# Performance work log

Hardware: AMD Instinct MI355X
Metric: run time of the kernel (lower is better)

## Reference

```python
import jax, jax.numpy as jnp
import numpy as np

B, T, C, H = 8, 2048, 1024, 128  # batch, seq (== block_size), n_embd, head_size


def setup_inputs() -> dict:
    key = jax.random.key(0)
    ks = jax.random.split(key, 4)
    s = 1.0 / np.sqrt(C)  # keep logits sane for softmax
    return {
        "embedded_data": jax.random.normal(ks[0], (B, T, C), dtype=jnp.float32),
        "Wq": jax.random.normal(ks[1], (C, H), dtype=jnp.float32) * s,
        "bq": jnp.zeros((H,), dtype=jnp.float32),
        "Wk": jax.random.normal(ks[2], (C, H), dtype=jnp.float32) * s,
        "bk": jnp.zeros((H,), dtype=jnp.float32),
        "Wv": jax.random.normal(ks[3], (C, H), dtype=jnp.float32) * s,
        "bv": jnp.zeros((H,), dtype=jnp.float32),
    }


def reference(embedded_data, Wq, bq, Wk, bk, Wv, bv):
    Bc, Tc, Cc = embedded_data.shape
    q = embedded_data @ Wq + bq                      # [B,T,H]
    k = embedded_data @ Wk + bk                      # [B,T,H]
    v = embedded_data @ Wv + bv                      # [B,T,H]
    # NOTE: source scales by C**-0.5 (input embed dim), not head_size**-0.5
    wei = jnp.einsum("bqh,bkh->bqk", q, k) * (Cc ** -0.5)  # [B,T,T]
    causal = jnp.tril(jnp.ones((Tc, Tc), dtype=bool))
    wei = jnp.where(causal, wei, -jnp.inf)
    wei = jax.nn.softmax(wei, axis=-1)
    # dropout(p=0.2) is identity in eval mode
    out = jnp.einsum("bqk,bkh->bqh", wei, v)         # [B,T,H]
    return out
```

## Files before the change

### kernel.cpp

```cpp
#include <hip/hip_runtime.h>
#include <cstdint>
#include <cstddef>

typedef __bf16 bf16x8 __attribute__((ext_vector_type(8)));
typedef float f32x4 __attribute__((ext_vector_type(4)));

#define B_ 8
#define T_ 2048
#define C_ 1024
#define H_ 128

#define QSC 0.045084220027780106f

__device__ __forceinline__ unsigned short f2bf(float f) {
    __bf16 h = (__bf16)f;
    return *(unsigned short*)&h;
}
__device__ __forceinline__ float bf2f(unsigned short u) {
    union { unsigned int i; float f; } x; x.i = ((unsigned int)u) << 16;
    return x.f;
}

__device__ __forceinline__ void gload16(void* lds, const void* g) {
    __builtin_amdgcn_global_load_lds(
        (const __attribute__((address_space(1))) unsigned int*)g,
        (__attribute__((address_space(3))) unsigned int*)lds, 16, 0, 0);
}

__global__ __launch_bounds__(256) void prep_w(
    const float* __restrict__ Wq, const float* __restrict__ Wk,
    const float* __restrict__ Wv, unsigned short* __restrict__ wt)
{
    int gid = blockIdx.x * 256 + threadIdx.x;
    int which = gid >> 14;
    int rem = gid & 16383;
    int n = rem >> 7;
    int kc = rem & 127;
    const float* W = which == 0 ? Wq : (which == 1 ? Wk : Wv);
    unsigned short tmp[8];
    #pragma unroll
    for (int i = 0; i < 8; ++i) tmp[i] = f2bf(W[(size_t)(kc * 8 + i) * H_ + n]);
    *(uint4*)&wt[((size_t)which * H_ + n) * C_ + kc * 8] = *(uint4*)tmp;
}

__global__ __launch_bounds__(256) void proj_kernel(
    const float* __restrict__ x, const unsigned short* __restrict__ wt,
    const float* __restrict__ bq, const float* __restrict__ bk,
    const float* __restrict__ bv,
    unsigned short* __restrict__ qo, unsigned short* __restrict__ ko,
    unsigned short* __restrict__ vo)
{
    const int which = blockIdx.y;
    const float* bias = which == 0 ? bq : (which == 1 ? bk : bv);

    __shared__ float xs[2][64 * 64];
    __shared__ unsigned short ws2[2][128 * 64];

    const int tid = threadIdx.x;
    const int w = tid >> 6, l = tid & 63, g = l >> 4, lc = l & 15;
    const int wm = w & 1, wn = w >> 1;
    const int m0 = blockIdx.x * 64;

    const unsigned short* wbase = &wt[(size_t)which * H_ * C_];

    f32x4 acc[2][4];
    #pragma unroll
    for (int im = 0; im < 2; ++im)
        #pragma unroll
        for (int jn = 0; jn < 4; ++jn) acc[im][jn] = f32x4{0.f, 0.f, 0.f, 0.f};

    auto stage = [&](int buf, int kc2) {
        const int kb = kc2 * 64;
        #pragma unroll
        for (int jj = 0; jj < 4; ++jj) {
            int slot = w * 256 + jj * 64 + l;
            int r = slot >> 3, cs = slot & 7;
            gload16(&ws2[buf][(w * 256 + jj * 64) * 8],
                    &wbase[(size_t)r * C_ + kb + ((cs ^ (r & 7)) * 8)]);
        }
        #pragma unroll
        for (int jj = 0; jj < 4; ++jj) {
            int slot = w * 256 + jj * 64 + l;
            int r = slot >> 4, cs = slot & 15;
            gload16(&xs[buf][(w * 256 + jj * 64) * 4],
                    &x[(size_t)(m0 + r) * C_ + kb + ((cs ^ (r & 15)) * 4)]);
        }
    };

    stage(0, 0);
    __syncthreads();

    int cur = 0;
    for (int kc = 0; kc < 16; ++kc) {
        if (kc < 15) stage(cur ^ 1, kc + 1);
        #pragma unroll
        for (int ks = 0; ks < 2; ++ks) {
            bf16x8 a[2], b[4];
            #pragma unroll
            for (int im = 0; im < 2; ++im) {
                int row = wm * 32 + im * 16 + lc;
                int u0 = ks * 8 + g * 2;
                f32x4 lo = *(const f32x4*)&xs[cur][(row * 16 + (u0 ^ (row & 15))) * 4];
                f32x4 hi = *(const f32x4*)&xs[cur][(row * 16 + ((u0 + 1) ^ (row & 15))) * 4];
                bf16x8 af;
                af[0] = (__bf16)lo[0]; af[1] = (__bf16)lo[1];
                af[2] = (__bf16)lo[2]; af[3] = (__bf16)lo[3];
                af[4] = (__bf16)hi[0]; af[5] = (__bf16)hi[1];
                af[6] = (__bf16)hi[2]; af[7] = (__bf16)hi[3];
                a[im] = af;
            }
            #pragma unroll
            for (int jn = 0; jn < 4; ++jn) {
                int n = wn * 64 + jn * 16 + lc;
                b[jn] = *(const bf16x8*)&ws2[cur][(n * 8 + ((ks * 4 + g) ^ (n & 7))) * 8];
            }
            #pragma unroll
            for (int im = 0; im < 2; ++im)
                #pragma unroll
                for (int jn = 0; jn < 4; ++jn)
                    acc[im][jn] = __builtin_amdgcn_mfma_f32_16x16x32_bf16(
                        a[im], b[jn], acc[im][jn], 0, 0, 0);
        }
        __syncthreads();
        cur ^= 1;
    }

    unsigned short* eb = (unsigned short*)&xs[0][0];
    if (which != 2) {
        const float osc = (which == 0) ? QSC : 1.0f;
        #pragma unroll
        for (int jn = 0; jn < 4; ++jn) {
            int n = wn * 64 + jn * 16 + lc;
            float bval = bias[n];
            #pragma unroll
            for (int im = 0; im < 2; ++im)
                #pragma unroll
                for (int r = 0; r < 4; ++r) {
                    int ml = wm * 32 + im * 16 + g * 4 + r;
                    eb[ml * 128 + n] = f2bf((acc[im][jn][r] + bval) * osc);
                }
        }
        __syncthreads();
        unsigned short* o = which == 0 ? qo : ko;
        #pragma unroll
        for (int i = 0; i < 4; ++i) {
            int cidx = i * 256 + tid;
            int row = cidx >> 4, c16 = cidx & 15;
            *(uint4*)&o[(size_t)(m0 + row) * H_ + c16 * 8] =
                *(const uint4*)&eb[row * 128 + c16 * 8];
        }
    } else {
        #pragma unroll
        for (int jn = 0; jn < 4; ++jn) {
            int n = wn * 64 + jn * 16 + lc;
            float bval = bias[n];
            #pragma unroll
            for (int im = 0; im < 2; ++im)
                #pragma unroll
                for (int r = 0; r < 4; ++r) {
                    int ml = wm * 32 + im * 16 + g * 4 + r;
                    eb[n * 64 + ml] = f2bf(acc[im][jn][r] + bval);
                }
        }
        __syncthreads();
        const int bi = m0 >> 11, t0 = m0 & (T_ - 1);
        #pragma unroll
        for (int i = 0; i < 4; ++i) {
            int cidx = i * 256 + tid;
            int n = cidx >> 3, cc = cidx & 7;
            *(uint4*)&vo[((size_t)(bi * H_ + n)) * T_ + t0 + cc * 8] =
                *(const uint4*)&eb[n * 64 + cc * 8];
        }
    }
}

__device__ __forceinline__ int pasc(int qt) {
    int m = qt >> 2, j = qt & 3;
    return 2 * m * (m + 1) + j * (m + 1);
}

__global__ __launch_bounds__(256, 2) void attn_split7(
    const unsigned short* __restrict__ q,
    const unsigned short* __restrict__ k,
    const unsigned short* __restrict__ vT,
    float* __restrict__ out,
    unsigned short* __restrict__ Opart, float* __restrict__ lws)
{
    const int bb = blockIdx.x;
    const int jj = 143 - (int)blockIdx.y;
    int qt = 31;
    while (pasc(qt) > jj) --qt;
    const int c = jj - pasc(qt);
    const int nch = (qt >> 2) + 1;
    const int q0 = qt * 64;
    const int kstart = c * 256;
    const int kend = min(kstart + 256, q0 + 64);
    const int ntiles = (kend - kstart) >> 5;

    const unsigned short* qb = q  + (size_t)bb * T_ * H_;
    const unsigned short* kb = k  + (size_t)bb * T_ * H_;
    const unsigned short* vb = vT + (size_t)bb * H_ * T_;

    __shared__ unsigned short Ks[2][32 * 128];
    __shared__ unsigned short Vs[2][128 * 32];
    __shared__ unsigned short Ps[4][16 * 64];

    const int tid = threadIdx.x;
    const int w = tid >> 6, l = tid & 63, gl = l >> 4, lc = l & 15;
    const int rowbase = q0 + w * 16;

    bf16x8 aq[4];
    #pragma unroll
    for (int ds = 0; ds < 4; ++ds)
        aq[ds] = *(const bf16x8*)&qb[(size_t)(rowbase + lc) * H_ + ds * 32 + gl * 8];

    f32x4 o[8];
    #pragma unroll
    for (int jo = 0; jo < 8; ++jo) o[jo] = f32x4{0.f, 0.f, 0.f, 0.f};
    float l_acc[4];
    #pragma unroll
    for (int r = 0; r < 4; ++r) l_acc[r] = 0.f;

    auto stageK = [&](int buf, int t) {
        const int kv0 = kstart + t * 32;
        #pragma unroll
        for (int ji = 0; ji < 2; ++ji) {
            int slot = (w * 2 + ji) * 64 + l;
            int r = slot >> 4, cs = slot & 15;
            gload16(&Ks[buf][((w * 2 + ji) * 64) * 8],
                    &kb[(size_t)(kv0 + r) * H_ + ((cs ^ (r & 7)) * 8)]);
        }
    };
    auto stageV = [&](int buf, int t) {
        const int kv0 = kstart + t * 32;
        #pragma unroll
        for (int ji = 0; ji < 2; ++ji) {
            int slot = (w * 2 + ji) * 64 + l;
            int r = slot >> 2, cs = slot & 3;
            gload16(&Vs[buf][((w * 2 + ji) * 64) * 8],
                    &vb[(size_t)r * T_ + kv0 + ((cs ^ (r & 3)) * 8)]);
        }
    };

    stageK(0, 0);
    stageV(0, 0);
    __syncthreads();

    int cur = 0;
    for (int t = 0; t < ntiles; ++t) {
        if (t + 1 < ntiles) { stageK(cur ^ 1, t + 1); stageV(cur ^ 1, t + 1); }
        const int kv0 = kstart + t * 32;
        const bool active = kv0 < rowbase + 16;
        if (active) {
            f32x4 s[2];
            #pragma unroll
            for (int jk = 0; jk < 2; ++jk) s[jk] = f32x4{0.f, 0.f, 0.f, 0.f};
            #pragma unroll
            for (int ds = 0; ds < 4; ++ds) {
                #pragma unroll
                for (int jk = 0; jk < 2; ++jk) {
                    int row = jk * 16 + lc;
                    bf16x8 kf = *(const bf16x8*)&Ks[cur][(row * 16 + ((ds * 4 + gl) ^ (row & 7))) * 8];
                    s[jk] = __builtin_amdgcn_mfma_f32_16x16x32_bf16(aq[ds], kf, s[jk], 0, 0, 0);
                }
            }
            if (kv0 + 31 > rowbase) {
                #pragma unroll
                for (int jk = 0; jk < 2; ++jk)
                    #pragma unroll
                    for (int r = 0; r < 4; ++r)
                        if (kv0 + jk * 16 + lc > rowbase + gl * 4 + r) s[jk][r] = -1e30f;
            }
            #pragma unroll
            for (int jk = 0; jk < 2; ++jk)
                #pragma unroll
                for (int r = 0; r < 4; ++r) {
                    float p = exp2f(fminf(s[jk][r], 80.f));
                    s[jk][r] = p;
                    l_acc[r] += p;
                }
            #pragma unroll
            for (int jk = 0; jk < 2; ++jk)
                #pragma unroll
                for (int r = 0; r < 4; ++r) {
                    int row = gl * 4 + r;
                    Ps[w][(row * 64 + jk * 16 + lc) ^ ((row & 7) << 3)] = f2bf(s[jk][r]);
                }
            {
                bf16x8 pa = *(const bf16x8*)&Ps[w][(lc * 64 + gl * 8) ^ ((lc & 7) << 3)];
                #pragma unroll
                for (int jo = 0; jo < 8; ++jo) {
                    int d = jo * 16 + lc;
                    bf16x8 vf = *(const bf16x8*)&Vs[cur][(d * 4 + (gl ^ (d & 3))) * 8];
                    o[jo] = __builtin_amdgcn_mfma_f32_16x16x32_bf16(pa, vf, o[jo], 0, 0, 0);
                }
            }
        }
        __syncthreads();
        cur ^= 1;
    }

    #pragma unroll
    for (int off = 1; off < 16; off <<= 1)
        #pragma unroll
        for (int r = 0; r < 4; ++r)
            l_acc[r] += __shfl_xor(l_acc[r], off, 64);

    if (nch == 1) {
        float* ob = out + (size_t)bb * T_ * H_;
        float inv[4];
        #pragma unroll
        for (int r = 0; r < 4; ++r) inv[r] = 1.0f / l_acc[r];
        #pragma unroll
        for (int jo = 0; jo < 8; ++jo)
            #pragma unroll
            for (int r = 0; r < 4; ++r)
                ob[(size_t)(rowbase + gl * 4 + r) * H_ + jo * 16 + lc] = o[jo][r] * inv[r];
    } else {
        const int slot = bb * 140 + (pasc(qt) - 4 + c);
        unsigned short* op = Opart + (size_t)slot * 8192;
        #pragma unroll
        for (int jo = 0; jo < 8; ++jo)
            #pragma unroll
            for (int r = 0; r < 4; ++r)
                op[(w * 16 + gl * 4 + r) * 128 + jo * 16 + lc] = f2bf(o[jo][r]);
        if (lc == 0) {
            #pragma unroll
            for (int r = 0; r < 4; ++r)
                lws[slot * 64 + w * 16 + gl * 4 + r] = l_acc[r];
        }
    }
}

__global__ __launch_bounds__(256) void combine_kernel(
    const unsigned short* __restrict__ Opart, const float* __restrict__ lws,
    float* __restrict__ out)
{
    const int rowid = blockIdx.x * 4 + (threadIdx.x >> 6);
    const int lane = threadIdx.x & 63;
    const int bb = rowid / 1792;
    const int t = 256 + (rowid - bb * 1792);
    const int qt = t >> 6;
    const int m = qt >> 2;
    const int nch = m + 1;
    const int p0 = 2 * m * (m + 1) + (qt & 3) * (m + 1);
    const int base = bb * 140 + (p0 - 4);
    const int r64 = t & 63;

    float L = 0.f, a0 = 0.f, a1 = 0.f;
    #pragma unroll
    for (int c2 = 0; c2 < 8; ++c2)
        if (c2 < nch) {
            L += lws[(base + c2) * 64 + r64];
            ushort2 uv = *(const ushort2*)&Opart[(size_t)(base + c2) * 8192 + r64 * 128 + lane * 2];
            a0 += bf2f(uv.x); a1 += bf2f(uv.y);
        }
    const float invL = 1.0f / L;
    *(float2*)&out[((size_t)bb * T_ + t) * H_ + lane * 2] = make_float2(a0 * invL, a1 * invL);
}

__global__ __launch_bounds__(128) void attn_mono(
    const unsigned short* __restrict__ q,
    const unsigned short* __restrict__ k,
    const unsigned short* __restrict__ vT,
    float* __restrict__ out)
{
    const int qt = (gridDim.x - 1) - blockIdx.x;
    const int bb = blockIdx.y;
    const int q0 = qt * 32;
    const unsigned short* qb = q  + (size_t)bb * T_ * H_;
    const unsigned short* kb = k  + (size_t)bb * T_ * H_;
    const unsigned short* vb = vT + (size_t)bb * H_ * T_;

    __shared__ unsigned short Ps[2][16 * 64];

    const int tid = threadIdx.x;
    const int w = tid >> 6, l = tid & 63, gl = l >> 4, lc = l & 15;

    bf16x8 aq[4];
    #pragma unroll
    for (int ds = 0; ds < 4; ++ds)
        aq[ds] = *(const bf16x8*)&qb[(size_t)(q0 + w * 16 + lc) * H_ + ds * 32 + gl * 8];

    f32x4 o[8];
    #pragma unroll
    for (int jo = 0; jo < 8; ++jo) o[jo] = f32x4{0.f, 0.f, 0.f, 0.f};
    float m_run[4], l_run[4];
    #pragma unroll
    for (int r = 0; r < 4; ++r) { m_run[r] = -INFINITY; l_run[r] = 0.f; }

    const int nt = (q0 >> 6) + 1;
    for (int t = 0; t < nt; ++t) {
        const int kv0 = t * 64;
        f32x4 s[4];
        #pragma unroll
        for (int jk = 0; jk < 4; ++jk) s[jk] = f32x4{0.f, 0.f, 0.f, 0.f};
        #pragma unroll
        for (int ds = 0; ds < 4; ++ds)
            #pragma unroll
            for (int jk = 0; jk < 4; ++jk) {
                bf16x8 bf = *(const bf16x8*)&kb[(size_t)(kv0 + jk * 16 + lc) * H_ + ds * 32 + gl * 8];
                s[jk] = __builtin_amdgcn_mfma_f32_16x16x32_bf16(aq[ds], bf, s[jk], 0, 0, 0);
            }
        if (kv0 + 63 > q0) {
            const int rowg = q0 + w * 16 + gl * 4;
            #pragma unroll
            for (int jk = 0; jk < 4; ++jk)
                #pragma unroll
                for (int r = 0; r < 4; ++r)
                    if (kv0 + jk * 16 + lc > rowg + r) s[jk][r] = -1e30f;
        }
        float pm[4];
        #pragma unroll
        for (int r = 0; r < 4; ++r)
            pm[r] = fmaxf(fmaxf(s[0][r], s[1][r]), fmaxf(s[2][r], s[3][r]));
        #pragma unroll
        for (int off = 1; off < 16; off <<= 1)
            #pragma unroll
            for (int r = 0; r < 4; ++r)
                pm[r] = fmaxf(pm[r], __shfl_xor(pm[r], off, 64));
        float scl[4], rs[4];
        #pragma unroll
        for (int r = 0; r < 4; ++r) {
            float mn = fmaxf(m_run[r], pm[r]);
            scl[r] = exp2f(m_run[r] - mn);
            m_run[r] = mn;
            rs[r] = 0.f;
        }
        #pragma unroll
        for (int jk = 0; jk < 4; ++jk)
            #pragma unroll
            for (int r = 0; r < 4; ++r) {
                float p = exp2f(s[jk][r] - m_run[r]);
                s[jk][r] = p;
                rs[r] += p;
            }
        #pragma unroll
        for (int off = 1; off < 16; off <<= 1)
            #pragma unroll
            for (int r = 0; r < 4; ++r)
                rs[r] += __shfl_xor(rs[r], off, 64);
        #pragma unroll
        for (int r = 0; r < 4; ++r)
            l_run[r] = l_run[r] * scl[r] + rs[r];
        #pragma unroll
        for (int jo = 0; jo < 8; ++jo)
            #pragma unroll
            for (int r = 0; r < 4; ++r)
                o[jo][r] *= scl[r];
        #pragma unroll
        for (int jk = 0; jk < 4; ++jk)
            #pragma unroll
            for (int r = 0; r < 4; ++r) {
                int row = gl * 4 + r;
                Ps[w][(row * 64 + jk * 16 + lc) ^ ((row & 7) << 3)] = f2bf(s[jk][r]);
            }
        #pragma unroll
        for (int ks = 0; ks < 2; ++ks) {
            bf16x8 pa = *(const bf16x8*)&Ps[w][(lc * 64 + ks * 32 + gl * 8) ^ ((lc & 7) << 3)];
            #pragma unroll
            for (int jo = 0; jo < 8; ++jo) {
                bf16x8 bv_ = *(const bf16x8*)&vb[(size_t)(jo * 16 + lc) * T_ + kv0 + ks * 32 + gl * 8];
                o[jo] = __builtin_amdgcn_mfma_f32_16x16x32_bf16(pa, bv_, o[jo], 0, 0, 0);
            }
        }
    }
    float* ob = out + (size_t)bb * T_ * H_;
    #pragma unroll
    for (int jo = 0; jo < 8; ++jo)
        #pragma unroll
        for (int r = 0; r < 4; ++r)
            ob[(size_t)(q0 + w * 16 + gl * 4 + r) * H_ + jo * 16 + lc] = o[jo][r] / l_run[r];
}

extern "C" void kernel_launch(void* const* d_in, const int* in_sizes, int n_in,
                              void* d_out, int out_size, void* d_ws, size_t ws_size,
                              hipStream_t stream) {
    const float* x  = (const float*)d_in[0];
    const float* Wq = (const float*)d_in[1];
    const float* bq = (const float*)d_in[2];
    const float* Wk = (const float*)d_in[3];
    const float* bk = (const float*)d_in[4];
    const float* Wv = (const float*)d_in[5];
    const float* bv = (const float*)d_in[6];
    float* out = (float*)d_out;

    const size_t qkv = (size_t)B_ * T_ * H_;
    unsigned short* qws = (unsigned short*)d_ws;
    unsigned short* kws = qws + qkv;
    unsigned short* vws = kws + qkv;
    unsigned short* wtw = vws + qkv;
    const size_t base_bytes = (3 * qkv + (size_t)3 * H_ * C_) * 2;
    unsigned short* Opart = (unsigned short*)((char*)d_ws + base_bytes);
    float* lws = (float*)((char*)d_ws + base_bytes + (size_t)1120 * 8192 * 2);
    const size_t need = base_bytes + (size_t)1120 * 8192 * 2 + (size_t)1120 * 64 * 4;

    prep_w<<<dim3(192), 256, 0, stream>>>(Wq, Wk, Wv, wtw);
    proj_kernel<<<dim3(256, 3), 256, 0, stream>>>(x, wtw, bq, bk, bv, qws, kws, vws);
    if (ws_size >= need) {
        attn_split7<<<dim3(8, 144), 256, 0, stream>>>(qws, kws, vws, out, Opart, lws);
        combine_kernel<<<dim3(3584), 256, 0, stream>>>(Opart, lws, out);
    } else {
        attn_mono<<<dim3(64, 8), 128, 0, stream>>>(qws, kws, vws, out);
    }
}
```

Baseline: 80.11 us.

## Fuse Q/K/V projections into one kernel sharing each x tile

Replaces the three-way grid over Q, K and V with a single 512-thread block that computes all 384 output columns for a 64-row tile of x. Each x tile is loaded from global memory and converted to bf16 once instead of three times. The block is larger and there are only 256 blocks instead of 768, and the V transpose now reads from LDS with strided scalar accesses. Fewer blocks may underfill the GPU and reduce latency hiding.

New measurement: 74.24 us. 1.08x faster.

```diff
diff --git a/kernel.cpp b/kernel.cpp
--- a/kernel.cpp
+++ b/kernel.cpp
@@ -43,46 +43,40 @@
     *(uint4*)&wt[((size_t)which * H_ + n) * C_ + kc * 8] = *(uint4*)tmp;
 }
 
-__global__ __launch_bounds__(256) void proj_kernel(
+__global__ __launch_bounds__(512, 2) void proj_fused(
     const float* __restrict__ x, const unsigned short* __restrict__ wt,
     const float* __restrict__ bq, const float* __restrict__ bk,
     const float* __restrict__ bv,
     unsigned short* __restrict__ qo, unsigned short* __restrict__ ko,
     unsigned short* __restrict__ vo)
 {
-    const int which = blockIdx.y;
-    const float* bias = which == 0 ? bq : (which == 1 ? bk : bv);
-
     __shared__ float xs[2][64 * 64];
-    __shared__ unsigned short ws2[2][128 * 64];
+    __shared__ unsigned short ws2[2][384 * 64];
 
     const int tid = threadIdx.x;
-    const int w = tid >> 6, l = tid & 63, g = l >> 4, lc = l & 15;
-    const int wm = w & 1, wn = w >> 1;
+    const int w = tid >> 6, l = tid & 63, gl = l >> 4, lc = l & 15;
+    const int rb = (w >> 1) * 16;
+    const int cb = (w & 1) * 192;
     const int m0 = blockIdx.x * 64;
 
-    const unsigned short* wbase = &wt[(size_t)which * H_ * C_];
-
-    f32x4 acc[2][4];
-    #pragma unroll
-    for (int im = 0; im < 2; ++im)
-        #pragma unroll
-        for (int jn = 0; jn < 4; ++jn) acc[im][jn] = f32x4{0.f, 0.f, 0.f, 0.f};
+    f32x4 acc[12];
+    #pragma unroll
+    for (int jn = 0; jn < 12; ++jn) acc[jn] = f32x4{0.f, 0.f, 0.f, 0.f};
 
     auto stage = [&](int buf, int kc2) {
         const int kb = kc2 * 64;
         #pragma unroll
-        for (int jj = 0; jj < 4; ++jj) {
-            int slot = w * 256 + jj * 64 + l;
-            int r = slot >> 3, cs = slot & 7;
-            gload16(&ws2[buf][(w * 256 + jj * 64) * 8],
-                    &wbase[(size_t)r * C_ + kb + ((cs ^ (r & 7)) * 8)]);
-        }
-        #pragma unroll
-        for (int jj = 0; jj < 4; ++jj) {
-            int slot = w * 256 + jj * 64 + l;
+        for (int ji = 0; ji < 6; ++ji) {
+            int slot = ji * 512 + tid;
+            int R = slot >> 3, cs = slot & 7;
+            gload16(&ws2[buf][(ji * 512 + w * 64) * 8],
+                    &wt[(size_t)R * C_ + kb + ((cs ^ (R & 7)) * 8)]);
+        }
+        #pragma unroll
+        for (int ji = 0; ji < 2; ++ji) {
+            int slot = ji * 512 + tid;
             int r = slot >> 4, cs = slot & 15;
-            gload16(&xs[buf][(w * 256 + jj * 64) * 4],
+            gload16(&xs[buf][(ji * 512 + w * 64) * 4],
                     &x[(size_t)(m0 + r) * C_ + kb + ((cs ^ (r & 15)) * 4)]);
         }
     };
@@ -95,81 +89,59 @@
         if (kc < 15) stage(cur ^ 1, kc + 1);
         #pragma unroll
         for (int ks = 0; ks < 2; ++ks) {
-            bf16x8 a[2], b[4];
-            #pragma unroll
-            for (int im = 0; im < 2; ++im) {
-                int row = wm * 32 + im * 16 + lc;
-                int u0 = ks * 8 + g * 2;
-                f32x4 lo = *(const f32x4*)&xs[cur][(row * 16 + (u0 ^ (row & 15))) * 4];
-                f32x4 hi = *(const f32x4*)&xs[cur][(row * 16 + ((u0 + 1) ^ (row & 15))) * 4];
-                bf16x8 af;
-                af[0] = (__bf16)lo[0]; af[1] = (__bf16)lo[1];
-                af[2] = (__bf16)lo[2]; af[3] = (__bf16)lo[3];
-                af[4] = (__bf16)hi[0]; af[5] = (__bf16)hi[1];
-                af[6] = (__bf16)hi[2]; af[7] = (__bf16)hi[3];
-                a[im] = af;
-            }
-            #pragma unroll
-            for (int jn = 0; jn < 4; ++jn) {
-                int n = wn * 64 + jn * 16 + lc;
-                b[jn] = *(const bf16x8*)&ws2[cur][(n * 8 + ((ks * 4 + g) ^ (n & 7))) * 8];
-            }
-            #pragma unroll
-            for (int im = 0; im < 2; ++im)
-                #pragma unroll
-                for (int jn = 0; jn < 4; ++jn)
-                    acc[im][jn] = __builtin_amdgcn_mfma_f32_16x16x32_bf16(
-                        a[im], b[jn], acc[im][jn], 0, 0, 0);
+            const int row = rb + lc;
+            const int u0 = ks * 8 + gl * 2;
+            f32x4 lo = *(const f32x4*)&xs[cur][(row * 16 + (u0 ^ (row & 15))) * 4];
+            f32x4 hi = *(const f32x4*)&xs[cur][(row * 16 + ((u0 + 1) ^ (row & 15))) * 4];
+            bf16x8 af;
+            af[0] = (__bf16)lo[0]; af[1] = (__bf16)lo[1];
+            af[2] = (__bf16)lo[2]; af[3] = (__bf16)lo[3];
+            af[4] = (__bf16)hi[0]; af[5] = (__bf16)hi[1];
+            af[6] = (__bf16)hi[2]; af[7] = (__bf16)hi[3];
+            #pragma unroll
+            for (int jn = 0; jn < 12; ++jn) {
+                int R = cb + jn * 16 + lc;
+                bf16x8 bfr = *(const bf16x8*)&ws2[cur][(R * 8 + ((ks * 4 + gl) ^ (R & 7))) * 8];
+                acc[jn] = __builtin_amdgcn_mfma_f32_16x16x32_bf16(af, bfr, acc[jn], 0, 0, 0);
+            }
         }
         __syncthreads();
         cur ^= 1;
     }
 
-    unsigned short* eb = (unsigned short*)&xs[0][0];
-    if (which != 2) {
-        const float osc = (which == 0) ? QSC : 1.0f;
-        #pragma unroll
-        for (int jn = 0; jn < 4; ++jn) {
-            int n = wn * 64 + jn * 16 + lc;
-            float bval = bias[n];
-            #pragma unroll
-            for (int im = 0; im < 2; ++im)
-                #pragma unroll
-                for (int r = 0; r < 4; ++r) {
-                    int ml = wm * 32 + im * 16 + g * 4 + r;
-                    eb[ml * 128 + n] = f2bf((acc[im][jn][r] + bval) * osc);
-                }
-        }
-        __syncthreads();
-        unsigned short* o = which == 0 ? qo : ko;
-        #pragma unroll
-        for (int i = 0; i < 4; ++i) {
-            int cidx = i * 256 + tid;
-            int row = cidx >> 4, c16 = cidx & 15;
-            *(uint4*)&o[(size_t)(m0 + row) * H_ + c16 * 8] =
-                *(const uint4*)&eb[row * 128 + c16 * 8];
-        }
-    } else {
-        #pragma unroll
-        for (int jn = 0; jn < 4; ++jn) {
-            int n = wn * 64 + jn * 16 + lc;
-            float bval = bias[n];
-            #pragma unroll
-            for (int im = 0; im < 2; ++im)
-                #pragma unroll
-                for (int r = 0; r < 4; ++r) {
-                    int ml = wm * 32 + im * 16 + g * 4 + r;
-                    eb[n * 64 + ml] = f2bf(acc[im][jn][r] + bval);
-                }
-        }
-        __syncthreads();
-        const int bi = m0 >> 11, t0 = m0 & (T_ - 1);
-        #pragma unroll
-        for (int i = 0; i < 4; ++i) {
-            int cidx = i * 256 + tid;
-            int n = cidx >> 3, cc = cidx & 7;
-            *(uint4*)&vo[((size_t)(bi * H_ + n)) * T_ + t0 + cc * 8] =
-                *(const uint4*)&eb[n * 64 + cc * 8];
+    unsigned short* eb = (unsigned short*)&ws2[0][0];
+    #pragma unroll
+    for (int jn = 0; jn < 12; ++jn) {
+        int n = cb + jn * 16 + lc;
+        int wh = n >> 7, nl = n & 127;
+        float bb = (wh == 0) ? bq[nl] : (wh == 1 ? bk[nl] : bv[nl]);
+        float sc = (wh == 0) ? QSC : 1.0f;
+        #pragma unroll
+        for (int r = 0; r < 4; ++r) {
+            int row = rb + gl * 4 + r;
+            eb[row * 392 + n] = f2bf((acc[jn][r] + bb) * sc);
+        }
+    }
+    __syncthreads();
+
+    const int bi = m0 >> 11, t0 = m0 & (T_ - 1);
+    #pragma unroll
+    for (int i = 0; i < 2; ++i) {
+        int c = i * 512 + tid;
+        {
+            int row = c >> 4, c16 = c & 15;
+            *(uint4*)&qo[(size_t)(m0 + row) * H_ + c16 * 8] =
+                *(const uint4*)&eb[row * 392 + c16 * 8];
+            *(uint4*)&ko[(size_t)(m0 + row) * H_ + c16 * 8] =
+                *(const uint4*)&eb[row * 392 + 128 + c16 * 8];
+        }
+        {
+            int n = c >> 3, cc = c & 7;
+            unsigned short tmp[8];
+            #pragma unroll
+            for (int ii = 0; ii < 8; ++ii)
+                tmp[ii] = eb[(cc * 8 + ii) * 392 + 256 + n];
+            *(uint4*)&vo[((size_t)(bi * H_ + n)) * T_ + t0 + cc * 8] = *(uint4*)tmp;
         }
     }
 }
@@ -496,7 +468,7 @@
     const size_t need = base_bytes + (size_t)1120 * 8192 * 2 + (size_t)1120 * 64 * 4;
 
     prep_w<<<dim3(192), 256, 0, stream>>>(Wq, Wk, Wv, wtw);
-    proj_kernel<<<dim3(256, 3), 256, 0, stream>>>(x, wtw, bq, bk, bv, qws, kws, vws);
+    proj_fused<<<dim3(256), 512, 0, stream>>>(x, wtw, bq, bk, bv, qws, kws, vws);
     if (ws_size >= need) {
         attn_split7<<<dim3(8, 144), 256, 0, stream>>>(qws, kws, vws, out, Opart, lws);
         combine_kernel<<<dim3(3584), 256, 0, stream>>>(Opart, lws, out);
```
